# Kernel tuning notes

Measured on AMD Instinct MI355X. Metric: run time of the kernel, lower is better.

The kernel has to match this reference:

```python
import jax, jax.numpy as jnp
import numpy as np

B, T, C = 4, 4096, 1024


def setup_inputs() -> dict:
    key = jax.random.key(0)
    k_x, k_f, k_g, k_p = jax.random.split(key, 4)
    scale = 1.0 / np.sqrt(C)  # keep gate pre-activations well-scaled
    return {
        "x": jax.random.normal(k_x, (B, T, C), dtype=jnp.float32),
        "W_f_x": jax.random.normal(k_f, (C, C), dtype=jnp.float32) * scale,
        "W_g_x": jax.random.normal(k_g, (C, C), dtype=jnp.float32) * scale,
        "W_proj": jax.random.normal(k_p, (C, C), dtype=jnp.float32) * scale,
    }


def _cfc_scan(a, b):
    """Solve h_t = a_t * h_{t-1} + b_t with h_{-1}=0 along axis 1 (T).

    Associative op on linear maps: (A_l,B_l) then (A_r,B_r) composes to
    (A_r*A_l, A_r*B_l + B_r). With h_init=0, h_t = B-component.
    """
    def op(l, r):
        al, bl = l
        ar, br = r
        return ar * al, ar * bl + br
    _, h = jax.lax.associative_scan(op, (a, b), axis=1)
    return h


def reference(x, W_f_x, W_g_x, W_proj):
    # Gates depend on x only (parallel mode). nn.Linear: x @ W.T
    f = jax.nn.sigmoid(jnp.einsum("btc,dc->btd", x, W_f_x))  # (B,T,C)
    g = jnp.tanh(jnp.einsum("btc,dc->btd", x, W_g_x))        # (B,T,C)
    h = _cfc_scan(f, (1.0 - f) * g)                           # (B,T,C)
    return jnp.einsum("btc,dc->btd", h, W_proj)               # c_proj
```

## Files before the change

### kernel.cpp

```cpp
#include <hip/hip_runtime.h>
#include <hip/hip_bf16.h>
#include <stdint.h>

#define TT 4096
#define BB 4
#define CC 1024
#define MM (BB * TT)
#define NCHUNK 128
#define CHUNK_T (TT / NCHUNK)
#define NCHAIN (BB * CC)

typedef float f32x4 __attribute__((ext_vector_type(4)));
typedef __bf16 bf16x8 __attribute__((ext_vector_type(8)));

__device__ __forceinline__ float b2f(ushort u) {
  union { float f; uint32_t v; } x; x.v = ((uint32_t)u) << 16; return x.f;
}
__device__ __forceinline__ ushort f2b(float f) {
  union { float f; uint32_t u; } x; x.f = f;
  uint32_t r = x.u + 0x7fffu + ((x.u >> 16) & 1u);
  return (ushort)(r >> 16);
}

__device__ __forceinline__ void async_copy16(const ushort* g, ushort* l) {
  __builtin_amdgcn_global_load_lds(
      (__attribute__((address_space(1))) void*)(g),
      (__attribute__((address_space(3))) void*)(l), 16, 0, 0);
}

__global__ __launch_bounds__(256) void cvt_all(const float* __restrict__ x,
                                               const float* __restrict__ wf,
                                               const float* __restrict__ wg,
                                               const float* __restrict__ wp,
                                               ushort* __restrict__ xb,
                                               ushort* __restrict__ wcat,
                                               ushort* __restrict__ wpb) {
  const int i = blockIdx.x * 256 + threadIdx.x;
  const float* s; ushort* d; int off;
  if (i < 4194304)            { s = x;  d = xb;              off = i; }
  else if (i < 4456448)       { s = wf; d = wcat;            off = i - 4194304; }
  else if (i < 4718592)       { s = wg; d = wcat + 1048576;  off = i - 4456448; }
  else                        { s = wp; d = wpb;             off = i - 4718592; }
  float4 v = ((const float4*)s)[off];
  ushort4 o;
  o.x = f2b(v.x); o.y = f2b(v.y); o.z = f2b(v.z); o.w = f2b(v.w);
  ((ushort4*)d)[off] = o;
}


#define RD_A(dst, slotoff, ih)                                          \
  _Pragma("unroll") for (int i_ = 0; i_ < 4; ++i_)                      \
      dst[i_] = *(const bf16x8*)(rA + (slotoff) + ((ih)*4 + i_) * 512);

#define RD_B(dst, slotoff)                                              \
  _Pragma("unroll") for (int j_ = 0; j_ < 4; ++j_)                      \
      dst[j_] = *(const bf16x8*)(rB + (slotoff) + j_ * 512);

#define MM_HALF(afb, bfb, ih)                                           \
  __builtin_amdgcn_s_setprio(1);                                        \
  _Pragma("unroll") for (int i_ = 0; i_ < 4; ++i_)                      \
  _Pragma("unroll") for (int j_ = 0; j_ < 4; ++j_)                      \
      acc[(ih)*4 + i_][j_] = __builtin_amdgcn_mfma_f32_16x16x32_bf16(   \
          bfb[j_], afb[i_], acc[(ih)*4 + i_][j_], 0, 0, 0);             \
  __builtin_amdgcn_s_setprio(0);

#define CKPT(n)                                                         \
  asm volatile("s_waitcnt vmcnt(" #n ")" ::: "memory");                 \
  __builtin_amdgcn_s_barrier();                                         \
  __builtin_amdgcn_sched_barrier(0);

#define TILE_BODY(s, ns, ss, ts, bfrC, bfrN, DO_STAGE, CKN)             \
  RD_A(afY, (s) * 8192, 1);                                             \
  if (DO_STAGE) stage((ss), (ts));                                      \
  MM_HALF(afX, bfrC, 0);                                                \
  CKPT(CKN);                                                            \
  RD_A(afX, (ns) * 8192, 0);                                            \
  RD_B(bfrN, (ns) * 8192);                                              \
  MM_HALF(afY, bfrC, 1);

template <int MODE>
__global__ __launch_bounds__(512, 2) void gemm_bt(const ushort* __restrict__ A,
                                                  const ushort* __restrict__ Bw,
                                                  float* __restrict__ outF,
                                                  ushort* __restrict__ outB, int N) {
  constexpr int K = CC;
  __shared__ __align__(16) ushort sA[4 * 256 * 32];
  __shared__ __align__(16) ushort sB[4 * 256 * 32];

  const int tid = threadIdx.x;
  const int lane = tid & 63;
  const int w = tid >> 6;
  const int wm = w >> 2;
  const int wn = w & 3;

  const int nbx = N >> 8;
  const int cpx = (int)gridDim.x >> 3;
  const int bid = blockIdx.x;
  const int wg = (bid & 7) * cpx + (bid >> 3);
  const long n0 = (long)(wg % nbx) << 8;
  const long m0 = (long)(wg / nbx) << 8;

  const int srow = lane >> 2;
  const int goct = (lane & 3) ^ ((lane >> 3) & 3);
  const ushort* gA0 = A + (m0 + w * 16 + srow) * K + goct * 8;
  const ushort* gB0 = Bw + (n0 + w * 16 + srow) * K + goct * 8;
  const ushort* gA1 = gA0 + 128 * (long)K;
  const ushort* gB1 = gB0 + 128 * (long)K;
  ushort* dA0 = &sA[w * 512 + lane * 8];
  ushort* dA1 = dA0 + 4096;
  ushort* dB0 = &sB[w * 512 + lane * 8];
  ushort* dB1 = dB0 + 4096;

  const int rlo = lane & 15;
  const int kq = lane >> 4;
  const int slot = kq ^ ((rlo >> 1) & 3);
  const ushort* rA = &sA[wm * 4096 + rlo * 32 + slot * 8];
  const ushort* rB = &sB[wn * 2048 + rlo * 32 + slot * 8];

  f32x4 acc[8][4];
#pragma unroll
  for (int i = 0; i < 8; ++i)
#pragma unroll
    for (int j = 0; j < 4; ++j) acc[i][j] = (f32x4){0.f, 0.f, 0.f, 0.f};

  auto stage = [&](int buf, int ts) {
    const int o = ts * 32;
    const int lo = buf * 8192;
    async_copy16(gA0 + o, dA0 + lo);
    async_copy16(gA1 + o, dA1 + lo);
    async_copy16(gB0 + o, dB0 + lo);
    async_copy16(gB1 + o, dB1 + lo);
  };

  bf16x8 afX[4], afY[4], bfrP[4], bfrQ[4];

  stage(0, 0);
  stage(1, 1);
  CKPT(4);
  RD_A(afX, 0, 0);
  RD_B(bfrP, 0);

  for (int t4 = 0; t4 < 7; ++t4) {
    const int tb = t4 * 4;
    TILE_BODY(0, 1, 2, tb + 2, bfrP, bfrQ, true, 4);
    TILE_BODY(1, 2, 3, tb + 3, bfrQ, bfrP, true, 4);
    TILE_BODY(2, 3, 0, tb + 4, bfrP, bfrQ, true, 4);
    TILE_BODY(3, 0, 1, tb + 5, bfrQ, bfrP, true, 4);
  }
  TILE_BODY(0, 1, 2, 30, bfrP, bfrQ, true, 4);
  TILE_BODY(1, 2, 3, 31, bfrQ, bfrP, true, 4);
  TILE_BODY(2, 3, 0, 0, bfrP, bfrQ, false, 0);
  RD_A(afY, 3 * 8192, 1);
  MM_HALF(afX, bfrQ, 0);
  MM_HALF(afY, bfrQ, 1);

  const int mloc = lane & 15;
  const int nq = (lane >> 4) * 4;
#pragma unroll
  for (int i = 0; i < 8; ++i) {
    const long m = m0 + wm * 128 + i * 16 + mloc;
#pragma unroll
    for (int j = 0; j < 4; ++j) {
      const long nb = n0 + wn * 64 + j * 16 + nq;
      const f32x4 v = acc[i][j];
      if (MODE == 0) {
        *(f32x4*)(outF + m * N + nb) = v;
      } else {
        float act[4];
        if (n0 < CC) {
#pragma unroll
          for (int r = 0; r < 4; ++r)
            act[r] = __builtin_amdgcn_rcpf(1.f + __expf(-v[r]));
        } else {
#pragma unroll
          for (int r = 0; r < 4; ++r)
            act[r] = fmaf(-2.f, __builtin_amdgcn_rcpf(1.f + __expf(2.f * v[r])), 1.f);
        }
        ushort4 o;
        o.x = f2b(act[0]); o.y = f2b(act[1]); o.z = f2b(act[2]); o.w = f2b(act[3]);
        *(ushort4*)(outB + m * (long)N + nb) = o;
      }
    }
  }
}

__global__ __launch_bounds__(256) void scan_pass1(const ushort* __restrict__ P,
                                                  float* __restrict__ cA,
                                                  float* __restrict__ cB) {
  const int pc = blockIdx.x * 256 + threadIdx.x;
  const int chunk = blockIdx.y;
  const int b = pc >> 8, c4 = (pc & 255) * 4;
  const ushort4* p =
      (const ushort4*)(P + (size_t)(b * TT + chunk * CHUNK_T) * (2 * CC) + c4);
  float A[4] = {1.f, 1.f, 1.f, 1.f};
  float h[4] = {0.f, 0.f, 0.f, 0.f};
#pragma unroll 4
  for (int i = 0; i < CHUNK_T; ++i) {
    const ushort4 fu = p[0];
    const ushort4 gu = p[CC / 4];
    p += 2 * CC / 4;
    const float f[4] = {b2f(fu.x), b2f(fu.y), b2f(fu.z), b2f(fu.w)};
    const float g[4] = {b2f(gu.x), b2f(gu.y), b2f(gu.z), b2f(gu.w)};
#pragma unroll
    for (int r = 0; r < 4; ++r) {
      A[r] *= f[r];
      h[r] = fmaf(f[r], h[r], (1.f - f[r]) * g[r]);
    }
  }
  const int ci = chunk * NCHAIN + b * CC + c4;
  *(f32x4*)(cA + ci) = (f32x4){A[0], A[1], A[2], A[3]};
  *(f32x4*)(cB + ci) = (f32x4){h[0], h[1], h[2], h[3]};
}

__global__ __launch_bounds__(256) void scan_pass2(const float* __restrict__ cA,
                                                  const float* __restrict__ cB,
                                                  float* __restrict__ hinit) {
  const int chain = blockIdx.x * 256 + threadIdx.x;
  float h = 0.f;
  for (int j = 0; j < NCHUNK; ++j) {
    hinit[j * NCHAIN + chain] = h;
    h = fmaf(cA[j * NCHAIN + chain], h, cB[j * NCHAIN + chain]);
  }
}

__global__ __launch_bounds__(256) void scan_pass3(const ushort* __restrict__ P,
                                                  const float* __restrict__ hinit,
                                                  ushort* __restrict__ H) {
  const int pc = blockIdx.x * 256 + threadIdx.x;
  const int chunk = blockIdx.y;
  const int b = pc >> 8, c4 = (pc & 255) * 4;
  f32x4 hv = *(const f32x4*)(hinit + chunk * NCHAIN + b * CC + c4);
  float h[4] = {hv[0], hv[1], hv[2], hv[3]};
  const ushort4* p =
      (const ushort4*)(P + (size_t)(b * TT + chunk * CHUNK_T) * (2 * CC) + c4);
  ushort4* hp = (ushort4*)(H + (size_t)(b * TT + chunk * CHUNK_T) * CC + c4);
#pragma unroll 4
  for (int i = 0; i < CHUNK_T; ++i) {
    const ushort4 fu = p[0];
    const ushort4 gu = p[CC / 4];
    p += 2 * CC / 4;
    const float f[4] = {b2f(fu.x), b2f(fu.y), b2f(fu.z), b2f(fu.w)};
    const float g[4] = {b2f(gu.x), b2f(gu.y), b2f(gu.z), b2f(gu.w)};
    ushort4 o;
#pragma unroll
    for (int r = 0; r < 4; ++r)
      h[r] = fmaf(f[r], h[r], (1.f - f[r]) * g[r]);
    o.x = f2b(h[0]); o.y = f2b(h[1]); o.z = f2b(h[2]); o.w = f2b(h[3]);
    *hp = o;
    hp += CC / 4;
  }
}

extern "C" void kernel_launch(void* const* d_in, const int* in_sizes, int n_in,
                              void* d_out, int out_size, void* d_ws, size_t ws_size,
                              hipStream_t stream) {
  const float* x  = (const float*)d_in[0];
  const float* Wf = (const float*)d_in[1];
  const float* Wg = (const float*)d_in[2];
  const float* Wp = (const float*)d_in[3];

  char* ws = (char*)d_ws;
  ushort* xb   = (ushort*)(ws);
  ushort* Hb   = xb;
  ushort* Wcat = (ushort*)(ws + 33554432);
  ushort* Wpb  = (ushort*)(ws + 33554432 + 4194304);
  ushort* P    = (ushort*)(ws + 33554432 + 4194304 + 2097152);
  char* tail   = ws + 33554432 + 4194304 + 2097152 + 67108864;
  float* cA    = (float*)Wcat;
  float* cB    = (float*)(((char*)Wcat) + 2097152);
  float* hinit = (float*)(tail);
  (void)ws_size; (void)in_sizes; (void)n_in; (void)out_size;

  cvt_all<<<19456, 256, 0, stream>>>(x, Wf, Wg, Wp, xb, Wcat, Wpb);

  gemm_bt<1><<<512, 512, 0, stream>>>(xb, Wcat, nullptr, P, 2 * CC);

  dim3 gs(NCHAIN / 4 / 256, NCHUNK);
  scan_pass1<<<gs, 256, 0, stream>>>(P, cA, cB);
  scan_pass2<<<NCHAIN / 256, 256, 0, stream>>>(cA, cB, hinit);
  scan_pass3<<<gs, 256, 0, stream>>>(P, hinit, Hb);

  gemm_bt<0><<<256, 512, 0, stream>>>(Hb, Wpb, (float*)d_out, nullptr, CC);
}
```

Baseline: 268.3 us.

## Restructure GEMM main loop into barrier-phased ping-pong schedule with split A/B staging

Replaces the double-register-buffered tile body, which prefetched the next A/B fragments during MFMA, with a single fragment set and a phase schedule. Each half-tile does an LDS read, then issues split A or B global staging, then waits on a barrier plus lgkmcnt before the MFMA block, followed by another barrier. The intent is a ping-pong style interleave where waves alternate between memory and MFMA phases, and it also frees the registers used for the second fragment set. The cost is more barriers per K step and less software prefetch overlap inside each wave.

```diff
diff --git a/kernel.cpp b/kernel.cpp
--- a/kernel.cpp
+++ b/kernel.cpp
@@ -48,35 +48,39 @@
 }
 
 
-#define RD_A(dst, slotoff, ih)                                          \
-  _Pragma("unroll") for (int i_ = 0; i_ < 4; ++i_)                      \
-      dst[i_] = *(const bf16x8*)(rA + (slotoff) + ((ih)*4 + i_) * 512);
-
-#define RD_B(dst, slotoff)                                              \
-  _Pragma("unroll") for (int j_ = 0; j_ < 4; ++j_)                      \
-      dst[j_] = *(const bf16x8*)(rB + (slotoff) + j_ * 512);
-
-#define MM_HALF(afb, bfb, ih)                                           \
-  __builtin_amdgcn_s_setprio(1);                                        \
-  _Pragma("unroll") for (int i_ = 0; i_ < 4; ++i_)                      \
-  _Pragma("unroll") for (int j_ = 0; j_ < 4; ++j_)                      \
-      acc[(ih)*4 + i_][j_] = __builtin_amdgcn_mfma_f32_16x16x32_bf16(   \
-          bfb[j_], afb[i_], acc[(ih)*4 + i_][j_], 0, 0, 0);             \
-  __builtin_amdgcn_s_setprio(0);
-
-#define CKPT(n)                                                         \
-  asm volatile("s_waitcnt vmcnt(" #n ")" ::: "memory");                 \
-  __builtin_amdgcn_s_barrier();                                         \
-  __builtin_amdgcn_sched_barrier(0);
-
-#define TILE_BODY(s, ns, ss, ts, bfrC, bfrN, DO_STAGE, CKN)             \
-  RD_A(afY, (s) * 8192, 1);                                             \
-  if (DO_STAGE) stage((ss), (ts));                                      \
-  MM_HALF(afX, bfrC, 0);                                                \
-  CKPT(CKN);                                                            \
-  RD_A(afX, (ns) * 8192, 0);                                            \
-  RD_B(bfrN, (ns) * 8192);                                              \
-  MM_HALF(afY, bfrC, 1);
+#define RDA(sl, ih)                                                       \
+  _Pragma("unroll") for (int i_ = 0; i_ < 4; ++i_)                        \
+      af[i_] = *(const bf16x8*)(rA + (sl) * 8192 + (ih) * 2048 + i_ * 512);
+
+#define RDB(sl)                                                           \
+  _Pragma("unroll") for (int j_ = 0; j_ < 4; ++j_)                        \
+      bfr[j_] = *(const bf16x8*)(rB + (sl) * 8192 + j_ * 512);
+
+#define MFMA16(ih)                                                        \
+  __builtin_amdgcn_s_setprio(1);                                          \
+  _Pragma("unroll") for (int i_ = 0; i_ < 4; ++i_)                        \
+  _Pragma("unroll") for (int j_ = 0; j_ < 4; ++j_)                        \
+      acc[(ih) * 4 + i_][j_] = __builtin_amdgcn_mfma_f32_16x16x32_bf16(   \
+          bfr[j_], af[i_], acc[(ih) * 4 + i_][j_], 0, 0, 0);              \
+  __builtin_amdgcn_s_setprio(0)
+
+#define MIDBAR()                                                          \
+  __builtin_amdgcn_s_barrier();                                           \
+  asm volatile("s_waitcnt lgkmcnt(0)" ::: "memory");                      \
+  __builtin_amdgcn_sched_barrier(0)
+
+#define ENDBAR()                                                          \
+  __builtin_amdgcn_s_barrier();                                           \
+  __builtin_amdgcn_sched_barrier(0)
+
+#define CK4() asm volatile("s_waitcnt vmcnt(4)" ::: "memory")
+#define CK0() asm volatile("s_waitcnt vmcnt(0)" ::: "memory")
+
+#define TILE(S0, S1, NS0, NS1, KN)                                        \
+  RDA(S0, 0); RDB(S0); stageA(NS0, (KN));      MIDBAR(); MFMA16(0);        ENDBAR(); \
+  RDA(S0, 1);          stageB(NS0, (KN));      MIDBAR(); MFMA16(1); CK4(); ENDBAR(); \
+  RDA(S1, 0); RDB(S1); stageA(NS1, (KN) + 32); MIDBAR(); MFMA16(0);        ENDBAR(); \
+  RDA(S1, 1);          stageB(NS1, (KN) + 32); MIDBAR(); MFMA16(1); CK4(); ENDBAR();
 
 template <int MODE>
 __global__ __launch_bounds__(512, 2) void gemm_bt(const ushort* __restrict__ A,
@@ -111,11 +115,20 @@
   ushort* dB0 = &sB[w * 512 + lane * 8];
   ushort* dB1 = dB0 + 4096;
 
+  auto stageA = [&](int slot, int koff) {
+    async_copy16(gA0 + koff, dA0 + slot * 8192);
+    async_copy16(gA1 + koff, dA1 + slot * 8192);
+  };
+  auto stageB = [&](int slot, int koff) {
+    async_copy16(gB0 + koff, dB0 + slot * 8192);
+    async_copy16(gB1 + koff, dB1 + slot * 8192);
+  };
+
   const int rlo = lane & 15;
   const int kq = lane >> 4;
-  const int slot = kq ^ ((rlo >> 1) & 3);
-  const ushort* rA = &sA[wm * 4096 + rlo * 32 + slot * 8];
-  const ushort* rB = &sB[wn * 2048 + rlo * 32 + slot * 8];
+  const int oslot = kq ^ ((rlo >> 1) & 3);
+  const ushort* rA = &sA[(wm * 128 + rlo) * 32 + oslot * 8];
+  const ushort* rB = &sB[(wn * 64 + rlo) * 32 + oslot * 8];
 
   f32x4 acc[8][4];
 #pragma unroll
@@ -123,36 +136,25 @@
 #pragma unroll
     for (int j = 0; j < 4; ++j) acc[i][j] = (f32x4){0.f, 0.f, 0.f, 0.f};
 
-  auto stage = [&](int buf, int ts) {
-    const int o = ts * 32;
-    const int lo = buf * 8192;
-    async_copy16(gA0 + o, dA0 + lo);
-    async_copy16(gA1 + o, dA1 + lo);
-    async_copy16(gB0 + o, dB0 + lo);
-    async_copy16(gB1 + o, dB1 + lo);
-  };
-
-  bf16x8 afX[4], afY[4], bfrP[4], bfrQ[4];
-
-  stage(0, 0);
-  stage(1, 1);
-  CKPT(4);
-  RD_A(afX, 0, 0);
-  RD_B(bfrP, 0);
-
-  for (int t4 = 0; t4 < 7; ++t4) {
-    const int tb = t4 * 4;
-    TILE_BODY(0, 1, 2, tb + 2, bfrP, bfrQ, true, 4);
-    TILE_BODY(1, 2, 3, tb + 3, bfrQ, bfrP, true, 4);
-    TILE_BODY(2, 3, 0, tb + 4, bfrP, bfrQ, true, 4);
-    TILE_BODY(3, 0, 1, tb + 5, bfrQ, bfrP, true, 4);
-  }
-  TILE_BODY(0, 1, 2, 30, bfrP, bfrQ, true, 4);
-  TILE_BODY(1, 2, 3, 31, bfrQ, bfrP, true, 4);
-  TILE_BODY(2, 3, 0, 0, bfrP, bfrQ, false, 0);
-  RD_A(afY, 3 * 8192, 1);
-  MM_HALF(afX, bfrQ, 0);
-  MM_HALF(afY, bfrQ, 1);
+  bf16x8 af[4], bfr[4];
+
+  stageA(0, 0);
+  stageB(0, 0);
+  stageA(1, 32);
+  stageB(1, 32);
+  CK4();
+  ENDBAR();
+
+  for (int t2 = 0; t2 < 7; ++t2) {
+    const int kn = t2 * 128 + 64;
+    TILE(0, 1, 2, 3, kn);
+    TILE(2, 3, 0, 1, kn + 64);
+  }
+  TILE(0, 1, 2, 3, 960);
+  RDA(2, 0); RDB(2); MIDBAR(); MFMA16(0); ENDBAR();
+  RDA(2, 1);         MIDBAR(); MFMA16(1); CK0(); ENDBAR();
+  RDA(3, 0); RDB(3); MIDBAR(); MFMA16(0); ENDBAR();
+  RDA(3, 1);         MIDBAR(); MFMA16(1);
 
   const int mloc = lane & 15;
   const int nq = (lane >> 4) * 4;
```

New measurement: 280.7 us. 4.6% more time.
